# Kernel tuning notes

Measured on AMD Instinct MI355X. Metric: run time of the kernel, lower is better.

The kernel has to match this reference:

```python
import jax, jax.numpy as jnp
import numpy as np

B, V, D = 256, 4096, 64

def setup_inputs() -> dict:
    key = jax.random.key(0)
    k1, k2 = jax.random.split(key)
    fusion_fs = jax.random.normal(k1, (B, V, D), dtype=jnp.float32)
    lan_fs = jax.random.normal(k2, (B, 1, D), dtype=jnp.float32)
    return {"fusion_fs": fusion_fs, "lan_fs": lan_fs}

def reference(fusion_fs, lan_fs):
    # sim_map: [b, a, q=1, v]
    sim = jnp.einsum('avd,bqd->baqv', fusion_fs, lan_fs)
    top2, _ = jax.lax.top_k(sim, 2)          # [B, B, 1, 2], sorted descending
    top2 = jnp.squeeze(top2, axis=2)          # [B, B, 2]  (q == 1)
    max_sim_0 = top2[..., 0]                  # [B, B]
    max_sim_1 = top2[..., 1]                  # [B, B]
    b = max_sim_0.shape[0]
    # off-diagonal selection of max_sim_1 -> [B, B-1], row-major order
    i = jnp.arange(b)[:, None]
    j = jnp.arange(b - 1)[None, :]
    max_sim_1_off = max_sim_1[i, j + (j >= i)]
    logits = jnp.concatenate([max_sim_0, max_sim_1_off], axis=1)  # [B, 2B-1]
    # target_pred = argmax(eye) = arange(B); CE with mean reduction
    logp = jax.nn.log_softmax(logits, axis=1)
    labels = jnp.arange(b)
    loss = -jnp.mean(logp[labels, labels])
    return loss
```

## Files before the change

### kernel.cpp

```cpp
#include <hip/hip_runtime.h>
#include <math.h>

#define BB 256
#define VV 4096
#define DD 64
#define NCHUNK 32
#define CHBG 32768
#define CHBL 16384

typedef __attribute__((ext_vector_type(8))) _Float16 f16x8;
typedef __attribute__((ext_vector_type(2))) __fp16 fp16x2;
typedef __attribute__((ext_vector_type(4))) float f32x4;

__global__ __launch_bounds__(512) void topk_sim_kernel(
    const float* __restrict__ F, const float* __restrict__ lan,
    float* __restrict__ max0T, float* __restrict__ max1T)
{
  extern __shared__ __align__(16) char smem[];
  __shared__ float mrg[8][64][2];

  const int t = threadIdx.x;
  const int a = blockIdx.x;
  const int wave = t >> 6;
  const int lane = t & 63;
  const int cl = lane & 15;
  const int o  = lane >> 4;
  const int rg = wave >> 2;
  const int cg = wave & 3;

  const char* gFa = (const char*)(F + (size_t)a * VV * DD);

  float4 bu[4][2][2];
#pragma unroll
  for (int ct = 0; ct < 4; ++ct)
#pragma unroll
    for (int s = 0; s < 2; ++s) {
      const float* p = lan + (cg * 64 + ct * 16 + cl) * DD + s * 32 + o * 8;
      bu[ct][s][0] = *(const float4*)p;
      bu[ct][s][1] = *(const float4*)(p + 4);
    }
  f16x8 bf[4][2];
#pragma unroll
  for (int ct = 0; ct < 4; ++ct)
#pragma unroll
    for (int s = 0; s < 2; ++s) {
      union { f16x8 v; fp16x2 h[4]; } U;
      U.h[0] = __builtin_amdgcn_cvt_pkrtz(bu[ct][s][0].x, bu[ct][s][0].y);
      U.h[1] = __builtin_amdgcn_cvt_pkrtz(bu[ct][s][0].z, bu[ct][s][0].w);
      U.h[2] = __builtin_amdgcn_cvt_pkrtz(bu[ct][s][1].x, bu[ct][s][1].y);
      U.h[3] = __builtin_amdgcn_cvt_pkrtz(bu[ct][s][1].z, bu[ct][s][1].w);
      bf[ct][s] = U.v;
    }

  const int woff = ((((t & 15) >> 1) ^ ((t >> 4) & 7)) << 4) + (t & 1) * 8;
  const int wrow = (t >> 4) * 128;

#define LOADG(S0, S1, S2, S3, CH) {                                   \
    const char* _g = gFa + (size_t)(CH) * CHBG + 16 * t;              \
    S0 = *(const float4*)(_g);                                        \
    S1 = *(const float4*)(_g + 8192);                                 \
    S2 = *(const float4*)(_g + 16384);                                \
    S3 = *(const float4*)(_g + 24576); }

#define CVTW(S0, S1, S2, S3, BUFP) {                                  \
    char* _b = (BUFP) + wrow + woff;                                  \
    uint2 _w;                                                         \
    union { uint2 u; fp16x2 h[2]; } _c;                               \
    _c.h[0] = __builtin_amdgcn_cvt_pkrtz(S0.x, S0.y);                 \
    _c.h[1] = __builtin_amdgcn_cvt_pkrtz(S0.z, S0.w); _w = _c.u;      \
    *(uint2*)(_b) = _w;                                               \
    _c.h[0] = __builtin_amdgcn_cvt_pkrtz(S1.x, S1.y);                 \
    _c.h[1] = __builtin_amdgcn_cvt_pkrtz(S1.z, S1.w); _w = _c.u;      \
    *(uint2*)(_b + 4096) = _w;                                        \
    _c.h[0] = __builtin_amdgcn_cvt_pkrtz(S2.x, S2.y);                 \
    _c.h[1] = __builtin_amdgcn_cvt_pkrtz(S2.z, S2.w); _w = _c.u;      \
    *(uint2*)(_b + 8192) = _w;                                        \
    _c.h[0] = __builtin_amdgcn_cvt_pkrtz(S3.x, S3.y);                 \
    _c.h[1] = __builtin_amdgcn_cvt_pkrtz(S3.z, S3.w); _w = _c.u;      \
    *(uint2*)(_b + 12288) = _w; }

  float m0[4], m1[4];
#pragma unroll
  for (int ct = 0; ct < 4; ++ct) { m0[ct] = -INFINITY; m1[ct] = -INFINITY; }

  auto compute = [&](const char* buf) {
#pragma unroll
    for (int rt = 0; rt < 4; ++rt) {
      const int row = rg * 64 + rt * 16 + cl;
      const int rx = cl & 7;
      const char* lp = buf + row * 128;
      f16x8 a0 = *(const f16x8*)(lp + ((o ^ rx) << 4));
      f16x8 a1 = *(const f16x8*)(lp + (((4 + o) ^ rx) << 4));
#pragma unroll
      for (int ct = 0; ct < 4; ++ct) {
        f32x4 acc = {0.f, 0.f, 0.f, 0.f};
        acc = __builtin_amdgcn_mfma_f32_16x16x32_f16(a0, bf[ct][0], acc, 0, 0, 0);
        acc = __builtin_amdgcn_mfma_f32_16x16x32_f16(a1, bf[ct][1], acc, 0, 0, 0);
        float h1 = fmaxf(acc[0], acc[1]), q1 = fminf(acc[0], acc[1]);
        float h2 = fmaxf(acc[2], acc[3]), q2 = fminf(acc[2], acc[3]);
        float M0 = fmaxf(h1, h2);
        float M1 = fmaxf(fminf(h1, h2), fmaxf(q1, q2));
        float old0 = m0[ct];
        m0[ct] = fmaxf(old0, M0);
        m1[ct] = fmaxf(m1[ct], fmaxf(fminf(old0, M0), M1));
      }
    }
  };

  char* buf0 = smem;
  char* buf1 = smem + CHBL;

  float4 E0, E1, E2, E3, O0, O1, O2, O3;
  LOADG(E0, E1, E2, E3, 0)
  LOADG(O0, O1, O2, O3, 1)
  asm volatile("s_waitcnt vmcnt(4)" ::: "memory");
  CVTW(E0, E1, E2, E3, buf0)
  asm volatile("s_waitcnt lgkmcnt(0)" ::: "memory");
  __builtin_amdgcn_s_barrier();

#pragma unroll 1
  for (int q = 0; q < 15; ++q) {
    const int ch = 2 * q;
    LOADG(E0, E1, E2, E3, ch + 2)
    asm volatile("s_waitcnt vmcnt(4)" ::: "memory");
    __builtin_amdgcn_sched_barrier(0);
    CVTW(O0, O1, O2, O3, buf1)
    compute(buf0);
    asm volatile("s_waitcnt lgkmcnt(0)" ::: "memory");
    __builtin_amdgcn_s_barrier();
    LOADG(O0, O1, O2, O3, ch + 3)
    asm volatile("s_waitcnt vmcnt(4)" ::: "memory");
    __builtin_amdgcn_sched_barrier(0);
    CVTW(E0, E1, E2, E3, buf0)
    compute(buf1);
    asm volatile("s_waitcnt lgkmcnt(0)" ::: "memory");
    __builtin_amdgcn_s_barrier();
  }
  asm volatile("s_waitcnt vmcnt(0)" ::: "memory");
  __builtin_amdgcn_sched_barrier(0);
  CVTW(O0, O1, O2, O3, buf1)
  compute(buf0);
  asm volatile("s_waitcnt lgkmcnt(0)" ::: "memory");
  __builtin_amdgcn_s_barrier();
  compute(buf1);
#undef LOADG
#undef CVTW

#pragma unroll
  for (int ct = 0; ct < 4; ++ct) {
#pragma unroll
    for (int off = 16; off <= 32; off <<= 1) {
      float p0 = __shfl_xor(m0[ct], off);
      float p1 = __shfl_xor(m1[ct], off);
      float n1 = fmaxf(fminf(m0[ct], p0), fmaxf(m1[ct], p1));
      m0[ct] = fmaxf(m0[ct], p0);
      m1[ct] = n1;
    }
    if (lane < 16) {
      mrg[wave][ct * 16 + lane][0] = m0[ct];
      mrg[wave][ct * 16 + lane][1] = m1[ct];
    }
  }
  __syncthreads();

  if (t < BB) {
    const int cg2 = t >> 6, lc = t & 63;
    float a0 = mrg[cg2][lc][0],     a1 = mrg[cg2][lc][1];
    float b0 = mrg[4 + cg2][lc][0], b1 = mrg[4 + cg2][lc][1];
    float M0 = fmaxf(a0, b0);
    float M1 = fmaxf(fminf(a0, b0), fmaxf(a1, b1));
    max0T[a * BB + t] = M0;
    max1T[a * BB + t] = M1;
  }
}

__global__ __launch_bounds__(256) void lse_kernel(
    const float* __restrict__ max0T, const float* __restrict__ max1T,
    float* __restrict__ lossb)
{
  __shared__ float red[256];
  __shared__ float diag;
  const int b = blockIdx.x;
  const int t = threadIdx.x;
  float x0 = max0T[t * BB + b];
  float x1 = (t == b) ? -INFINITY : max1T[t * BB + b];
  if (t == b) diag = x0;
  red[t] = fmaxf(x0, x1);
  __syncthreads();
  for (int s = 128; s > 0; s >>= 1) {
    if (t < s) red[t] = fmaxf(red[t], red[t + s]);
    __syncthreads();
  }
  float M = red[0];
  __syncthreads();
  float e = expf(x0 - M) + ((t == b) ? 0.0f : expf(x1 - M));
  red[t] = e;
  __syncthreads();
  for (int s = 128; s > 0; s >>= 1) {
    if (t < s) red[t] = red[t] + red[t + s];
    __syncthreads();
  }
  if (t == 0) lossb[b] = logf(red[0]) + M - diag;
}

__global__ __launch_bounds__(256) void mean_kernel(
    const float* __restrict__ lossb, float* __restrict__ out)
{
  __shared__ float red[256];
  const int t = threadIdx.x;
  red[t] = lossb[t];
  __syncthreads();
  for (int s = 128; s > 0; s >>= 1) {
    if (t < s) red[t] += red[t + s];
    __syncthreads();
  }
  if (t == 0) out[0] = red[0] * (1.0f / 256.0f);
}

extern "C" void kernel_launch(void* const* d_in, const int* in_sizes, int n_in,
                              void* d_out, int out_size, void* d_ws, size_t ws_size,
                              hipStream_t stream) {
  const float* F   = (const float*)d_in[0];
  const float* lan = (const float*)d_in[1];
  float* ws = (float*)d_ws;
  float* max0T = ws;
  float* max1T = ws + 65536;
  float* lossb = ws + 131072;

  const int shmem = 2 * CHBL;
  topk_sim_kernel<<<256, 512, shmem, stream>>>(F, lan, max0T, max1T);
  lse_kernel<<<256, 256, 0, stream>>>(max0T, max1T, lossb);
  mean_kernel<<<1, 256, 0, stream>>>(lossb, (float*)d_out);
}
```

Before: 66.80 us.

## Split each sim row over two 256-thread blocks and merge top-2 partials in LSE

The top-k kernel now launches 512 blocks of 256 threads, each covering half of the V dimension for one row a, instead of 256 blocks of 512 threads. Each wave now holds 8 column tiles of the lan operand rather than 4, doubling reuse of each A fragment across MFMAs. The in-block shared-memory merge is dropped. Per-wave partial top-2 values go to a 4x larger workspace, and the LSE kernel folds the four partials per entry. The aim is more blocks to fill the CUs and fewer barriers, at the cost of more register pressure and extra global traffic for the partials.

```diff
diff --git a/kernel.cpp b/kernel.cpp
--- a/kernel.cpp
+++ b/kernel.cpp
@@ -5,52 +5,57 @@
 #define VV 4096
 #define DD 64
 #define NCHUNK 32
-#define CHBG 32768
-#define CHBL 16384
+#define CHBG 16384
+#define CHBL 8192
 
 typedef __attribute__((ext_vector_type(8))) _Float16 f16x8;
 typedef __attribute__((ext_vector_type(2))) __fp16 fp16x2;
 typedef __attribute__((ext_vector_type(4))) float f32x4;
 
-__global__ __launch_bounds__(512) void topk_sim_kernel(
+__global__ __launch_bounds__(256) void topk_sim_kernel(
     const float* __restrict__ F, const float* __restrict__ lan,
-    float* __restrict__ max0T, float* __restrict__ max1T)
+    float* __restrict__ max0P, float* __restrict__ max1P)
 {
   extern __shared__ __align__(16) char smem[];
-  __shared__ float mrg[8][64][2];
 
   const int t = threadIdx.x;
-  const int a = blockIdx.x;
+  const int a    = blockIdx.x >> 1;
+  const int half = blockIdx.x & 1;
   const int wave = t >> 6;
   const int lane = t & 63;
   const int cl = lane & 15;
   const int o  = lane >> 4;
-  const int rg = wave >> 2;
-  const int cg = wave & 3;
-
-  const char* gFa = (const char*)(F + (size_t)a * VV * DD);
-
-  float4 bu[4][2][2];
-#pragma unroll
-  for (int ct = 0; ct < 4; ++ct)
-#pragma unroll
-    for (int s = 0; s < 2; ++s) {
-      const float* p = lan + (cg * 64 + ct * 16 + cl) * DD + s * 32 + o * 8;
-      bu[ct][s][0] = *(const float4*)p;
-      bu[ct][s][1] = *(const float4*)(p + 4);
-    }
-  f16x8 bf[4][2];
-#pragma unroll
-  for (int ct = 0; ct < 4; ++ct)
-#pragma unroll
-    for (int s = 0; s < 2; ++s) {
-      union { f16x8 v; fp16x2 h[4]; } U;
-      U.h[0] = __builtin_amdgcn_cvt_pkrtz(bu[ct][s][0].x, bu[ct][s][0].y);
-      U.h[1] = __builtin_amdgcn_cvt_pkrtz(bu[ct][s][0].z, bu[ct][s][0].w);
-      U.h[2] = __builtin_amdgcn_cvt_pkrtz(bu[ct][s][1].x, bu[ct][s][1].y);
-      U.h[3] = __builtin_amdgcn_cvt_pkrtz(bu[ct][s][1].z, bu[ct][s][1].w);
-      bf[ct][s] = U.v;
-    }
+  const int rg = wave >> 1;
+  const int cg = wave & 1;
+
+  const char* gFa = (const char*)(F + (size_t)a * VV * DD
+                                  + (size_t)half * 2048 * DD);
+
+  f16x8 bf[8][2];
+#pragma unroll
+  for (int g = 0; g < 2; ++g) {
+    float4 bu4[4][2][2];
+#pragma unroll
+    for (int ci = 0; ci < 4; ++ci)
+#pragma unroll
+      for (int s = 0; s < 2; ++s) {
+        const float* p = lan + (cg * 128 + (g * 4 + ci) * 16 + cl) * DD
+                         + s * 32 + o * 8;
+        bu4[ci][s][0] = *(const float4*)p;
+        bu4[ci][s][1] = *(const float4*)(p + 4);
+      }
+#pragma unroll
+    for (int ci = 0; ci < 4; ++ci)
+#pragma unroll
+      for (int s = 0; s < 2; ++s) {
+        union { f16x8 v; fp16x2 h[4]; } U;
+        U.h[0] = __builtin_amdgcn_cvt_pkrtz(bu4[ci][s][0].x, bu4[ci][s][0].y);
+        U.h[1] = __builtin_amdgcn_cvt_pkrtz(bu4[ci][s][0].z, bu4[ci][s][0].w);
+        U.h[2] = __builtin_amdgcn_cvt_pkrtz(bu4[ci][s][1].x, bu4[ci][s][1].y);
+        U.h[3] = __builtin_amdgcn_cvt_pkrtz(bu4[ci][s][1].z, bu4[ci][s][1].w);
+        bf[g * 4 + ci][s] = U.v;
+      }
+  }
 
   const int woff = ((((t & 15) >> 1) ^ ((t >> 4) & 7)) << 4) + (t & 1) * 8;
   const int wrow = (t >> 4) * 128;
@@ -58,41 +63,40 @@
 #define LOADG(S0, S1, S2, S3, CH) {                                   \
     const char* _g = gFa + (size_t)(CH) * CHBG + 16 * t;              \
     S0 = *(const float4*)(_g);                                        \
-    S1 = *(const float4*)(_g + 8192);                                 \
-    S2 = *(const float4*)(_g + 16384);                                \
-    S3 = *(const float4*)(_g + 24576); }
+    S1 = *(const float4*)(_g + 4096);                                 \
+    S2 = *(const float4*)(_g + 8192);                                 \
+    S3 = *(const float4*)(_g + 12288); }
 
 #define CVTW(S0, S1, S2, S3, BUFP) {                                  \
     char* _b = (BUFP) + wrow + woff;                                  \
-    uint2 _w;                                                         \
     union { uint2 u; fp16x2 h[2]; } _c;                               \
     _c.h[0] = __builtin_amdgcn_cvt_pkrtz(S0.x, S0.y);                 \
-    _c.h[1] = __builtin_amdgcn_cvt_pkrtz(S0.z, S0.w); _w = _c.u;      \
-    *(uint2*)(_b) = _w;                                               \
+    _c.h[1] = __builtin_amdgcn_cvt_pkrtz(S0.z, S0.w);                 \
+    *(uint2*)(_b) = _c.u;                                             \
     _c.h[0] = __builtin_amdgcn_cvt_pkrtz(S1.x, S1.y);                 \
-    _c.h[1] = __builtin_amdgcn_cvt_pkrtz(S1.z, S1.w); _w = _c.u;      \
-    *(uint2*)(_b + 4096) = _w;                                        \
+    _c.h[1] = __builtin_amdgcn_cvt_pkrtz(S1.z, S1.w);                 \
+    *(uint2*)(_b + 2048) = _c.u;                                      \
     _c.h[0] = __builtin_amdgcn_cvt_pkrtz(S2.x, S2.y);                 \
-    _c.h[1] = __builtin_amdgcn_cvt_pkrtz(S2.z, S2.w); _w = _c.u;      \
-    *(uint2*)(_b + 8192) = _w;                                        \
+    _c.h[1] = __builtin_amdgcn_cvt_pkrtz(S2.z, S2.w);                 \
+    *(uint2*)(_b + 4096) = _c.u;                                      \
     _c.h[0] = __builtin_amdgcn_cvt_pkrtz(S3.x, S3.y);                 \
-    _c.h[1] = __builtin_amdgcn_cvt_pkrtz(S3.z, S3.w); _w = _c.u;      \
-    *(uint2*)(_b + 12288) = _w; }
-
-  float m0[4], m1[4];
-#pragma unroll
-  for (int ct = 0; ct < 4; ++ct) { m0[ct] = -INFINITY; m1[ct] = -INFINITY; }
+    _c.h[1] = __builtin_amdgcn_cvt_pkrtz(S3.z, S3.w);                 \
+    *(uint2*)(_b + 6144) = _c.u; }
+
+  float m0[8], m1[8];
+#pragma unroll
+  for (int ct = 0; ct < 8; ++ct) { m0[ct] = -INFINITY; m1[ct] = -INFINITY; }
 
   auto compute = [&](const char* buf) {
 #pragma unroll
-    for (int rt = 0; rt < 4; ++rt) {
-      const int row = rg * 64 + rt * 16 + cl;
+    for (int rt = 0; rt < 2; ++rt) {
+      const int row = rg * 32 + rt * 16 + cl;
       const int rx = cl & 7;
       const char* lp = buf + row * 128;
       f16x8 a0 = *(const f16x8*)(lp + ((o ^ rx) << 4));
       f16x8 a1 = *(const f16x8*)(lp + (((4 + o) ^ rx) << 4));
 #pragma unroll
-      for (int ct = 0; ct < 4; ++ct) {
+      for (int ct = 0; ct < 8; ++ct) {
         f32x4 acc = {0.f, 0.f, 0.f, 0.f};
         acc = __builtin_amdgcn_mfma_f32_16x16x32_f16(a0, bf[ct][0], acc, 0, 0, 0);
         acc = __builtin_amdgcn_mfma_f32_16x16x32_f16(a1, bf[ct][1], acc, 0, 0, 0);
@@ -147,7 +151,7 @@
 #undef CVTW
 
 #pragma unroll
-  for (int ct = 0; ct < 4; ++ct) {
+  for (int ct = 0; ct < 8; ++ct) {
 #pragma unroll
     for (int off = 16; off <= 32; off <<= 1) {
       float p0 = __shfl_xor(m0[ct], off);
@@ -157,33 +161,32 @@
       m1[ct] = n1;
     }
     if (lane < 16) {
-      mrg[wave][ct * 16 + lane][0] = m0[ct];
-      mrg[wave][ct * 16 + lane][1] = m1[ct];
+      const int col = cg * 128 + ct * 16 + lane;
+      max0P[((size_t)a * 4 + half * 2 + rg) * BB + col] = m0[ct];
+      max1P[((size_t)a * 4 + half * 2 + rg) * BB + col] = m1[ct];
     }
   }
-  __syncthreads();
-
-  if (t < BB) {
-    const int cg2 = t >> 6, lc = t & 63;
-    float a0 = mrg[cg2][lc][0],     a1 = mrg[cg2][lc][1];
-    float b0 = mrg[4 + cg2][lc][0], b1 = mrg[4 + cg2][lc][1];
-    float M0 = fmaxf(a0, b0);
-    float M1 = fmaxf(fminf(a0, b0), fmaxf(a1, b1));
-    max0T[a * BB + t] = M0;
-    max1T[a * BB + t] = M1;
-  }
 }
 
 __global__ __launch_bounds__(256) void lse_kernel(
-    const float* __restrict__ max0T, const float* __restrict__ max1T,
+    const float* __restrict__ max0P, const float* __restrict__ max1P,
     float* __restrict__ lossb)
 {
   __shared__ float red[256];
   __shared__ float diag;
   const int b = blockIdx.x;
   const int t = threadIdx.x;
-  float x0 = max0T[t * BB + b];
-  float x1 = (t == b) ? -INFINITY : max1T[t * BB + b];
+  float M0 = -INFINITY, M1 = -INFINITY;
+#pragma unroll
+  for (int q = 0; q < 4; ++q) {
+    float p0 = max0P[((size_t)t * 4 + q) * BB + b];
+    float p1 = max1P[((size_t)t * 4 + q) * BB + b];
+    float n1 = fmaxf(fminf(M0, p0), fmaxf(M1, p1));
+    M0 = fmaxf(M0, p0);
+    M1 = n1;
+  }
+  float x0 = M0;
+  float x1 = (t == b) ? -INFINITY : M1;
   if (t == b) diag = x0;
   red[t] = fmaxf(x0, x1);
   __syncthreads();
@@ -223,12 +226,12 @@
   const float* F   = (const float*)d_in[0];
   const float* lan = (const float*)d_in[1];
   float* ws = (float*)d_ws;
-  float* max0T = ws;
-  float* max1T = ws + 65536;
-  float* lossb = ws + 131072;
+  float* max0P = ws;
+  float* max1P = ws + 262144;
+  float* lossb = ws + 524288;
 
   const int shmem = 2 * CHBL;
-  topk_sim_kernel<<<256, 512, shmem, stream>>>(F, lan, max0T, max1T);
-  lse_kernel<<<256, 256, 0, stream>>>(max0T, max1T, lossb);
+  topk_sim_kernel<<<512, 256, shmem, stream>>>(F, lan, max0P, max1P);
+  lse_kernel<<<256, 256, 0, stream>>>(max0P, max1P, lossb);
   mean_kernel<<<1, 256, 0, stream>>>(lossb, (float*)d_out);
 }
```

Measured after the change: 79.33 us. 1.19x slower.
